# Optimization experiments

Hardware: AMD Instinct MI355X
Metric: run time of the kernel (lower is better)

The kernel has to match this reference:

```python
import jax, jax.numpy as jnp
import numpy as np

B, IN, OUT = 131072, 128, 32
GRID_SIZE, SPLINE_ORDER = 5, 3
GRID_LO, GRID_HI = -1.0, 1.0
N_BASIS = GRID_SIZE + SPLINE_ORDER  # 8


def _centers_and_spacing():
    n_knots = GRID_SIZE + 2 * SPLINE_ORDER + 1  # 12
    grid = jnp.linspace(GRID_LO, GRID_HI, n_knots)
    centers = grid[SPLINE_ORDER:SPLINE_ORDER + N_BASIS]  # (8,)
    spacing = (GRID_HI - GRID_LO) / GRID_SIZE + 1e-06
    return centers, spacing


def setup_inputs() -> dict:
    key = jax.random.key(0)
    k1, k2, k3 = jax.random.split(key, 3)
    x = jax.random.normal(k1, (B, IN), dtype=jnp.float32)
    coeff = jax.random.normal(k2, (IN, OUT, N_BASIS), dtype=jnp.float32) * 0.1
    base_weight = jnp.ones((IN, OUT), dtype=jnp.float32)
    base_bias = jnp.zeros((IN, OUT), dtype=jnp.float32)
    edge_weights = jax.random.normal(k3, (IN, OUT), dtype=jnp.float32) * 0.1
    return {"x": x, "coeff": coeff, "base_weight": base_weight,
            "base_bias": base_bias, "edge_weights": edge_weights}


def reference(x, coeff, base_weight, base_bias, edge_weights):
    # y[b,j] = sum_i w[i,j] * ( bw[i,j]*silu(x[b,i]) + bb[i,j]
    #                           + sum_k basis[b,i,k]*coeff[i,j,k] )
    centers, spacing = _centers_and_spacing()
    silu = x * jax.nn.sigmoid(x)                                    # (B, I)
    z = (x[:, :, None] - centers[None, None, :]) / spacing          # (B, I, K)
    basis = jnp.exp(-0.5 * z * z)                                   # (B, I, K)
    # base activation contribution
    base_out = jnp.einsum('bi,ij->bj', silu, edge_weights * base_weight)
    bias_out = jnp.sum(edge_weights * base_bias, axis=0)            # (J,)
    # spline contribution: contract over input dim i and basis dim k
    spline_out = jnp.einsum('bik,ijk->bj', basis,
                            edge_weights[:, :, None] * coeff)
    return base_out + bias_out[None, :] + spline_out
```

## Files before the change

kernel.cpp:

```cpp
#include <hip/hip_runtime.h>

typedef short bf16x8 __attribute__((ext_vector_type(8)));
typedef float f32x4v __attribute__((ext_vector_type(4)));

constexpr double H_D    = 0.4 + 1e-6;
constexpr double INVH_D = 1.0 / H_D;
constexpr double C0_D   = -1.0 + 6.0 / 11.0;
constexpr double DLT_D  = (2.0 / 11.0) / H_D;
constexpr double L2E_D  = 1.4426950408889634;

constexpr float INVH = (float)INVH_D;
constexpr float NC0H = (float)(-C0_D * INVH_D);
constexpr float A2f  = (float)(-0.5 * L2E_D);
constexpr float B2f  = (float)(DLT_D * L2E_D);
constexpr float GCF  = (float)(-0.5 * DLT_D * DLT_D * L2E_D);
constexpr float NL2E = (float)(-L2E_D);

__device__ __forceinline__ float fexp2(float v) {
#if __has_builtin(__builtin_amdgcn_exp2f)
  return __builtin_amdgcn_exp2f(v);
#else
  return exp2f(v);
#endif
}
__device__ __forceinline__ float frcp(float v) {
#if __has_builtin(__builtin_amdgcn_rcpf)
  return __builtin_amdgcn_rcpf(v);
#else
  return 1.0f / v;
#endif
}
__device__ __forceinline__ float siluf(float v) {
  return v * frcp(1.0f + fexp2(NL2E * v));
}
__device__ __forceinline__ unsigned pk2(float lo, float hi) {
  unsigned a = __float_as_uint(hi) + 0x8000u;
  unsigned b = __float_as_uint(lo) + 0x8000u;
  return __builtin_amdgcn_perm(a, b, 0x07060302u);
}
__device__ __forceinline__ bf16x8 packfrag(const float (&v)[8]) {
  uint4 d;
  d.x = pk2(v[0], v[1]);
  d.y = pk2(v[2], v[3]);
  d.z = pk2(v[4], v[5]);
  d.w = pk2(v[6], v[7]);
  return __builtin_bit_cast(bf16x8, d);
}
__device__ __forceinline__ unsigned rne16(float f) {
  unsigned u = __float_as_uint(f);
  return (u + 0x7fffu + ((u >> 16) & 1u)) >> 16;
}

__global__ void kan_prep(const float* __restrict__ coeff,
                         const float* __restrict__ bw,
                         const float* __restrict__ bb,
                         const float* __restrict__ ew,
                         uint4* __restrict__ wfrag,
                         float* __restrict__ bias) {
  if (blockIdx.x == 18) {
    int n = threadIdx.x;
    if (n < 32) {
      float s = 0.f;
      for (int i = 0; i < 128; ++i) s += ew[i * 32 + n] * bb[i * 32 + n];
      bias[n] = s;
    }
    return;
  }
  const int e    = blockIdx.x * 4 + (threadIdx.x >> 6);
  const int lane = threadIdx.x & 63;
  const int s = e >> 1, h = e & 1;
  const int G = s / 9, t = s % 9;
  const int n = h * 16 + (lane & 15);
  const int cbase = G * 32 + (lane >> 4) * 8;
  float v[8];
  if (t == 0) {
#pragma unroll
    for (int j = 0; j < 8; ++j) {
      int i = cbase + j;
      v[j] = ew[i * 32 + n] * bw[i * 32 + n];
    }
  } else {
    const int k = t - 1;
    const float g = exp2f(GCF * (float)(k * k));
#pragma unroll
    for (int j = 0; j < 8; ++j) {
      int i = cbase + j;
      v[j] = ew[i * 32 + n] * coeff[(i * 32 + n) * 8 + k] * g;
    }
  }
  uint4 d;
  d.x = (rne16(v[1]) << 16) | rne16(v[0]);
  d.y = (rne16(v[3]) << 16) | rne16(v[2]);
  d.z = (rne16(v[5]) << 16) | rne16(v[4]);
  d.w = (rne16(v[7]) << 16) | rne16(v[6]);
  wfrag[e * 64 + lane] = d;
}

__global__ __launch_bounds__(256, 2) void kan_main(
    const float* __restrict__ x,
    const uint4* __restrict__ wfrag,
    const float* __restrict__ bias,
    float* __restrict__ out) {
  const int lane = threadIdx.x & 63;
  const int wave = threadIdx.x >> 6;
  const int m    = lane & 15;
  const int quad = lane >> 4;
  const long rowbase = ((long)blockIdx.x * 4 + wave) * 64;

  f32x4v acc[4][2];
#pragma unroll
  for (int tl = 0; tl < 4; ++tl)
#pragma unroll
    for (int hh = 0; hh < 2; ++hh)
#pragma unroll
      for (int rr = 0; rr < 4; ++rr) acc[tl][hh][rr] = 0.f;

  const float* xbase = x + (long)m * 128 + quad * 8;

#pragma unroll
  for (int G = 0; G < 4; ++G) {
    const uint4* wf = wfrag + (size_t)G * 18 * 64 + lane;

    float xc[4][8];
#pragma unroll
    for (int tl = 0; tl < 4; ++tl) {
      const float4* p = reinterpret_cast<const float4*>(
          xbase + (rowbase + tl * 16) * 128 + G * 32);
      float4 a = p[0], b = p[1];
      xc[tl][0] = a.x; xc[tl][1] = a.y; xc[tl][2] = a.z; xc[tl][3] = a.w;
      xc[tl][4] = b.x; xc[tl][5] = b.y; xc[tl][6] = b.z; xc[tl][7] = b.w;
    }

    bf16x8 b0 = __builtin_bit_cast(bf16x8, wf[0]);
    bf16x8 b1 = __builtin_bit_cast(bf16x8, wf[64]);
#pragma unroll
    for (int tl = 0; tl < 4; ++tl) {
      float sv[8];
#pragma unroll
      for (int j = 0; j < 8; ++j) sv[j] = siluf(xc[tl][j]);
      bf16x8 af = packfrag(sv);
      acc[tl][0] = __builtin_amdgcn_mfma_f32_16x16x32_bf16(af, b0, acc[tl][0], 0, 0, 0);
      acc[tl][1] = __builtin_amdgcn_mfma_f32_16x16x32_bf16(af, b1, acc[tl][1], 0, 0, 0);
    }

    float pg[4][8], rg[4][8];
#pragma unroll
    for (int tl = 0; tl < 4; ++tl)
#pragma unroll
      for (int j = 0; j < 8; ++j) {
        float u = fmaf(xc[tl][j], INVH, NC0H);
        pg[tl][j] = fexp2(A2f * u * u);
        rg[tl][j] = fexp2(B2f * u);
      }

#pragma unroll
    for (int t = 1; t <= 8; ++t) {
      bf16x8 c0 = __builtin_bit_cast(bf16x8, wf[(t * 2) * 64]);
      bf16x8 c1 = __builtin_bit_cast(bf16x8, wf[(t * 2 + 1) * 64]);
#pragma unroll
      for (int tl = 0; tl < 4; ++tl) {
        bf16x8 af = packfrag(pg[tl]);
        acc[tl][0] = __builtin_amdgcn_mfma_f32_16x16x32_bf16(af, c0, acc[tl][0], 0, 0, 0);
        acc[tl][1] = __builtin_amdgcn_mfma_f32_16x16x32_bf16(af, c1, acc[tl][1], 0, 0, 0);
        if (t < 8) {
#pragma unroll
          for (int j = 0; j < 8; ++j) pg[tl][j] *= rg[tl][j];
        }
      }
    }
  }

  const float bv0 = bias[m];
  const float bv1 = bias[m + 16];
#pragma unroll
  for (int tl = 0; tl < 4; ++tl) {
#pragma unroll
    for (int rr = 0; rr < 4; ++rr) {
      long row = rowbase + tl * 16 + quad * 4 + rr;
      out[row * 32 + m]      = acc[tl][0][rr] + bv0;
      out[row * 32 + m + 16] = acc[tl][1][rr] + bv1;
    }
  }
}

extern "C" void kernel_launch(void* const* d_in, const int* in_sizes, int n_in,
                              void* d_out, int out_size, void* d_ws, size_t ws_size,
                              hipStream_t stream) {
  const float* x     = (const float*)d_in[0];
  const float* coeff = (const float*)d_in[1];
  const float* bw    = (const float*)d_in[2];
  const float* bb    = (const float*)d_in[3];
  const float* ew    = (const float*)d_in[4];

  uint4* wfrag = (uint4*)d_ws;
  float* bias  = (float*)((char*)d_ws + 73728);

  kan_prep<<<19, 256, 0, stream>>>(coeff, bw, bb, ew, wfrag, bias);
  kan_main<<<512, 256, 0, stream>>>(x, wfrag, bias, (float*)d_out);
}
```

Measured before the change: 127.5 us.

## Halve rows per wave, double grid, raise occupancy and prefetch next x chunk

Each wave now handles 32 rows instead of 64, the grid doubles to 1024 blocks, and launch bounds ask for 4 blocks per CU. The next group's x values are loaded into registers while the current group's MFMAs run. This targets load latency and low occupancy from the large per-thread register footprint. The cost is that each B weight fragment is reused across fewer row tiles, so weight loads per row double.

```diff
diff --git a/kernel.cpp b/kernel.cpp
--- a/kernel.cpp
+++ b/kernel.cpp
@@ -96,7 +96,7 @@
   wfrag[e * 64 + lane] = d;
 }
 
-__global__ __launch_bounds__(256, 2) void kan_main(
+__global__ __launch_bounds__(256, 4) void kan_main(
     const float* __restrict__ x,
     const uint4* __restrict__ wfrag,
     const float* __restrict__ bias,
@@ -105,60 +105,73 @@
   const int wave = threadIdx.x >> 6;
   const int m    = lane & 15;
   const int quad = lane >> 4;
-  const long rowbase = ((long)blockIdx.x * 4 + wave) * 64;
-
-  f32x4v acc[4][2];
-#pragma unroll
-  for (int tl = 0; tl < 4; ++tl)
+  const long rowbase = ((long)blockIdx.x * 4 + wave) * 32;
+
+  f32x4v acc[2][2];
+#pragma unroll
+  for (int tl = 0; tl < 2; ++tl)
 #pragma unroll
     for (int hh = 0; hh < 2; ++hh)
 #pragma unroll
       for (int rr = 0; rr < 4; ++rr) acc[tl][hh][rr] = 0.f;
 
-  const float* xbase = x + (long)m * 128 + quad * 8;
+  const float* xbase = x + (rowbase + m) * 128 + (long)quad * 8;
+
+  float xb[2][8];
+#pragma unroll
+  for (int tl = 0; tl < 2; ++tl) {
+    const float4* p =
+        reinterpret_cast<const float4*>(xbase + (long)tl * 16 * 128);
+    float4 a = p[0], b = p[1];
+    xb[tl][0] = a.x; xb[tl][1] = a.y; xb[tl][2] = a.z; xb[tl][3] = a.w;
+    xb[tl][4] = b.x; xb[tl][5] = b.y; xb[tl][6] = b.z; xb[tl][7] = b.w;
+  }
 
 #pragma unroll
   for (int G = 0; G < 4; ++G) {
     const uint4* wf = wfrag + (size_t)G * 18 * 64 + lane;
 
-    float xc[4][8];
-#pragma unroll
-    for (int tl = 0; tl < 4; ++tl) {
-      const float4* p = reinterpret_cast<const float4*>(
-          xbase + (rowbase + tl * 16) * 128 + G * 32);
-      float4 a = p[0], b = p[1];
-      xc[tl][0] = a.x; xc[tl][1] = a.y; xc[tl][2] = a.z; xc[tl][3] = a.w;
-      xc[tl][4] = b.x; xc[tl][5] = b.y; xc[tl][6] = b.z; xc[tl][7] = b.w;
-    }
-
-    bf16x8 b0 = __builtin_bit_cast(bf16x8, wf[0]);
-    bf16x8 b1 = __builtin_bit_cast(bf16x8, wf[64]);
-#pragma unroll
-    for (int tl = 0; tl < 4; ++tl) {
+    bf16x8 af0[2];
+    float pg[2][8], rg[2][8];
+#pragma unroll
+    for (int tl = 0; tl < 2; ++tl) {
       float sv[8];
 #pragma unroll
-      for (int j = 0; j < 8; ++j) sv[j] = siluf(xc[tl][j]);
-      bf16x8 af = packfrag(sv);
-      acc[tl][0] = __builtin_amdgcn_mfma_f32_16x16x32_bf16(af, b0, acc[tl][0], 0, 0, 0);
-      acc[tl][1] = __builtin_amdgcn_mfma_f32_16x16x32_bf16(af, b1, acc[tl][1], 0, 0, 0);
-    }
-
-    float pg[4][8], rg[4][8];
-#pragma unroll
-    for (int tl = 0; tl < 4; ++tl)
+      for (int j = 0; j < 8; ++j) sv[j] = siluf(xb[tl][j]);
+      af0[tl] = packfrag(sv);
 #pragma unroll
       for (int j = 0; j < 8; ++j) {
-        float u = fmaf(xc[tl][j], INVH, NC0H);
+        float u = fmaf(xb[tl][j], INVH, NC0H);
         pg[tl][j] = fexp2(A2f * u * u);
         rg[tl][j] = fexp2(B2f * u);
       }
+    }
+
+    if (G < 3) {
+#pragma unroll
+      for (int tl = 0; tl < 2; ++tl) {
+        const float4* p = reinterpret_cast<const float4*>(
+            xbase + (long)tl * 16 * 128 + (G + 1) * 32);
+        float4 a = p[0], b = p[1];
+        xb[tl][0] = a.x; xb[tl][1] = a.y; xb[tl][2] = a.z; xb[tl][3] = a.w;
+        xb[tl][4] = b.x; xb[tl][5] = b.y; xb[tl][6] = b.z; xb[tl][7] = b.w;
+      }
+    }
+
+    bf16x8 b0 = __builtin_bit_cast(bf16x8, wf[0]);
+    bf16x8 b1 = __builtin_bit_cast(bf16x8, wf[64]);
+#pragma unroll
+    for (int tl = 0; tl < 2; ++tl) {
+      acc[tl][0] = __builtin_amdgcn_mfma_f32_16x16x32_bf16(af0[tl], b0, acc[tl][0], 0, 0, 0);
+      acc[tl][1] = __builtin_amdgcn_mfma_f32_16x16x32_bf16(af0[tl], b1, acc[tl][1], 0, 0, 0);
+    }
 
 #pragma unroll
     for (int t = 1; t <= 8; ++t) {
       bf16x8 c0 = __builtin_bit_cast(bf16x8, wf[(t * 2) * 64]);
       bf16x8 c1 = __builtin_bit_cast(bf16x8, wf[(t * 2 + 1) * 64]);
 #pragma unroll
-      for (int tl = 0; tl < 4; ++tl) {
+      for (int tl = 0; tl < 2; ++tl) {
         bf16x8 af = packfrag(pg[tl]);
         acc[tl][0] = __builtin_amdgcn_mfma_f32_16x16x32_bf16(af, c0, acc[tl][0], 0, 0, 0);
         acc[tl][1] = __builtin_amdgcn_mfma_f32_16x16x32_bf16(af, c1, acc[tl][1], 0, 0, 0);
@@ -173,7 +186,7 @@
   const float bv0 = bias[m];
   const float bv1 = bias[m + 16];
 #pragma unroll
-  for (int tl = 0; tl < 4; ++tl) {
+  for (int tl = 0; tl < 2; ++tl) {
 #pragma unroll
     for (int rr = 0; rr < 4; ++rr) {
       long row = rowbase + tl * 16 + quad * 4 + rr;
@@ -196,5 +209,5 @@
   float* bias  = (float*)((char*)d_ws + 73728);
 
   kan_prep<<<19, 256, 0, stream>>>(coeff, bw, bb, ew, wfrag, bias);
-  kan_main<<<512, 256, 0, stream>>>(x, wfrag, bias, (float*)d_out);
-}
+  kan_main<<<1024, 256, 0, stream>>>(x, wfrag, bias, (float*)d_out);
+}
```

After: 121.7 us. -4.6%, faster.

## Stage weight fragments in LDS and shrink per-wave tile to raise occupancy

Applied to the files above, without the earlier changes.

The main kernel now gives each wave 16 rows instead of 64, launches four times as many blocks, and raises the launch bound to 8 blocks per SM. Each block copies the weight fragments for every input group into LDS with global_load_lds, and the next group's x values are prefetched while the current group is computed. The aim is more latency hiding through occupancy, and cheaper weight reads from LDS than repeated global reads. The cost is a barrier per group and weights reloaded by four times as many blocks, with less MFMA reuse of each weight fragment per wave. The bias reduction in the prep kernel is also parallelised across 256 threads.

```diff
diff --git a/kernel.cpp b/kernel.cpp
--- a/kernel.cpp
+++ b/kernel.cpp
@@ -58,11 +58,20 @@
                          uint4* __restrict__ wfrag,
                          float* __restrict__ bias) {
   if (blockIdx.x == 18) {
-    int n = threadIdx.x;
-    if (n < 32) {
-      float s = 0.f;
-      for (int i = 0; i < 128; ++i) s += ew[i * 32 + n] * bb[i * 32 + n];
-      bias[n] = s;
+    __shared__ float part[256];
+    const int n = threadIdx.x & 31;
+    const int c = threadIdx.x >> 5;
+    float s = 0.f;
+#pragma unroll
+    for (int i = c * 16; i < c * 16 + 16; ++i)
+      s += ew[i * 32 + n] * bb[i * 32 + n];
+    part[threadIdx.x] = s;
+    __syncthreads();
+    if (threadIdx.x < 32) {
+      float t = 0.f;
+#pragma unroll
+      for (int c2 = 0; c2 < 8; ++c2) t += part[c2 * 32 + threadIdx.x];
+      bias[threadIdx.x] = t;
     }
     return;
   }
@@ -96,90 +105,99 @@
   wfrag[e * 64 + lane] = d;
 }
 
-__global__ __launch_bounds__(256, 2) void kan_main(
+__device__ __forceinline__ void gl_lds16(const uint4* g, uint4* l) {
+  __builtin_amdgcn_global_load_lds(
+      (const __attribute__((address_space(1))) void*)g,
+      (__attribute__((address_space(3))) void*)l, 16, 0, 0);
+}
+
+__global__ __launch_bounds__(256, 8) void kan_main(
     const float* __restrict__ x,
     const uint4* __restrict__ wfrag,
     const float* __restrict__ bias,
     float* __restrict__ out) {
-  const int lane = threadIdx.x & 63;
-  const int wave = threadIdx.x >> 6;
+  __shared__ uint4 wlds[1152];
+  const int tid  = threadIdx.x;
+  const int lane = tid & 63;
+  const int wave = tid >> 6;
   const int m    = lane & 15;
   const int quad = lane >> 4;
-  const long rowbase = ((long)blockIdx.x * 4 + wave) * 64;
-
-  f32x4v acc[4][2];
-#pragma unroll
-  for (int tl = 0; tl < 4; ++tl)
-#pragma unroll
-    for (int hh = 0; hh < 2; ++hh)
-#pragma unroll
-      for (int rr = 0; rr < 4; ++rr) acc[tl][hh][rr] = 0.f;
-
-  const float* xbase = x + (long)m * 128 + quad * 8;
-
-#pragma unroll
-  for (int G = 0; G < 4; ++G) {
-    const uint4* wf = wfrag + (size_t)G * 18 * 64 + lane;
-
-    float xc[4][8];
-#pragma unroll
-    for (int tl = 0; tl < 4; ++tl) {
-      const float4* p = reinterpret_cast<const float4*>(
-          xbase + (rowbase + tl * 16) * 128 + G * 32);
-      float4 a = p[0], b = p[1];
-      xc[tl][0] = a.x; xc[tl][1] = a.y; xc[tl][2] = a.z; xc[tl][3] = a.w;
-      xc[tl][4] = b.x; xc[tl][5] = b.y; xc[tl][6] = b.z; xc[tl][7] = b.w;
-    }
-
-    bf16x8 b0 = __builtin_bit_cast(bf16x8, wf[0]);
-    bf16x8 b1 = __builtin_bit_cast(bf16x8, wf[64]);
-#pragma unroll
-    for (int tl = 0; tl < 4; ++tl) {
-      float sv[8];
-#pragma unroll
-      for (int j = 0; j < 8; ++j) sv[j] = siluf(xc[tl][j]);
-      bf16x8 af = packfrag(sv);
-      acc[tl][0] = __builtin_amdgcn_mfma_f32_16x16x32_bf16(af, b0, acc[tl][0], 0, 0, 0);
-      acc[tl][1] = __builtin_amdgcn_mfma_f32_16x16x32_bf16(af, b1, acc[tl][1], 0, 0, 0);
-    }
-
-    float pg[4][8], rg[4][8];
-#pragma unroll
-    for (int tl = 0; tl < 4; ++tl)
-#pragma unroll
-      for (int j = 0; j < 8; ++j) {
-        float u = fmaf(xc[tl][j], INVH, NC0H);
-        pg[tl][j] = fexp2(A2f * u * u);
-        rg[tl][j] = fexp2(B2f * u);
-      }
-
-#pragma unroll
-    for (int t = 1; t <= 8; ++t) {
-      bf16x8 c0 = __builtin_bit_cast(bf16x8, wf[(t * 2) * 64]);
-      bf16x8 c1 = __builtin_bit_cast(bf16x8, wf[(t * 2 + 1) * 64]);
-#pragma unroll
-      for (int tl = 0; tl < 4; ++tl) {
-        bf16x8 af = packfrag(pg[tl]);
-        acc[tl][0] = __builtin_amdgcn_mfma_f32_16x16x32_bf16(af, c0, acc[tl][0], 0, 0, 0);
-        acc[tl][1] = __builtin_amdgcn_mfma_f32_16x16x32_bf16(af, c1, acc[tl][1], 0, 0, 0);
-        if (t < 8) {
-#pragma unroll
-          for (int j = 0; j < 8; ++j) pg[tl][j] *= rg[tl][j];
-        }
-      }
-    }
-  }
-
+  const long rowbase = ((long)blockIdx.x * 4 + wave) * 16;
+
+  f32x4v acc0, acc1;
+#pragma unroll
+  for (int rr = 0; rr < 4; ++rr) { acc0[rr] = 0.f; acc1[rr] = 0.f; }
+
+  const float* xbase = x + (rowbase + m) * 128 + (long)quad * 8;
+
+  float xb[8];
+  {
+    const float4* p = reinterpret_cast<const float4*>(xbase);
+    float4 a = p[0], b = p[1];
+    xb[0] = a.x; xb[1] = a.y; xb[2] = a.z; xb[3] = a.w;
+    xb[4] = b.x; xb[5] = b.y; xb[6] = b.z; xb[7] = b.w;
+  }
   const float bv0 = bias[m];
   const float bv1 = bias[m + 16];
-#pragma unroll
-  for (int tl = 0; tl < 4; ++tl) {
-#pragma unroll
-    for (int rr = 0; rr < 4; ++rr) {
-      long row = rowbase + tl * 16 + quad * 4 + rr;
-      out[row * 32 + m]      = acc[tl][0][rr] + bv0;
-      out[row * 32 + m + 16] = acc[tl][1][rr] + bv1;
-    }
+
+#pragma unroll 1
+  for (int G = 0; G < 4; ++G) {
+    if (G) __syncthreads();
+    const uint4* src = wfrag + (size_t)G * 1152;
+#pragma unroll
+    for (int i = 0; i < 4; ++i)
+      gl_lds16(src + tid + i * 256, &wlds[tid + i * 256]);
+    if (tid < 128) gl_lds16(src + 1024 + tid, &wlds[1024 + tid]);
+    __syncthreads();
+
+    bf16x8 af0;
+    float pg[8], rg[8];
+    {
+      float sv[8];
+#pragma unroll
+      for (int j = 0; j < 8; ++j) sv[j] = siluf(xb[j]);
+      af0 = packfrag(sv);
+#pragma unroll
+      for (int j = 0; j < 8; ++j) {
+        float u = fmaf(xb[j], INVH, NC0H);
+        pg[j] = fexp2(A2f * u * u);
+        rg[j] = fexp2(B2f * u);
+      }
+    }
+
+    if (G < 3) {
+      const float4* p = reinterpret_cast<const float4*>(xbase + (G + 1) * 32);
+      float4 a = p[0], b = p[1];
+      xb[0] = a.x; xb[1] = a.y; xb[2] = a.z; xb[3] = a.w;
+      xb[4] = b.x; xb[5] = b.y; xb[6] = b.z; xb[7] = b.w;
+    }
+
+    const uint4* wl = wlds + lane;
+
+    acc0 = __builtin_amdgcn_mfma_f32_16x16x32_bf16(
+        af0, __builtin_bit_cast(bf16x8, wl[0]), acc0, 0, 0, 0);
+    acc1 = __builtin_amdgcn_mfma_f32_16x16x32_bf16(
+        af0, __builtin_bit_cast(bf16x8, wl[64]), acc1, 0, 0, 0);
+
+#pragma unroll
+    for (int t = 1; t <= 8; ++t) {
+      bf16x8 c0 = __builtin_bit_cast(bf16x8, wl[t * 128]);
+      bf16x8 c1 = __builtin_bit_cast(bf16x8, wl[t * 128 + 64]);
+      bf16x8 af = packfrag(pg);
+      acc0 = __builtin_amdgcn_mfma_f32_16x16x32_bf16(af, c0, acc0, 0, 0, 0);
+      acc1 = __builtin_amdgcn_mfma_f32_16x16x32_bf16(af, c1, acc1, 0, 0, 0);
+      if (t < 8) {
+#pragma unroll
+        for (int j = 0; j < 8; ++j) pg[j] *= rg[j];
+      }
+    }
+  }
+
+#pragma unroll
+  for (int rr = 0; rr < 4; ++rr) {
+    long row = rowbase + quad * 4 + rr;
+    out[row * 32 + m]      = acc0[rr] + bv0;
+    out[row * 32 + m + 16] = acc1[rr] + bv1;
   }
 }
 
@@ -196,5 +214,5 @@
   float* bias  = (float*)((char*)d_ws + 73728);
 
   kan_prep<<<19, 256, 0, stream>>>(coeff, bw, bb, ew, wfrag, bias);
-  kan_main<<<512, 256, 0, stream>>>(x, wfrag, bias, (float*)d_out);
-}
+  kan_main<<<2048, 256, 0, stream>>>(x, wfrag, bias, (float*)d_out);
+}
```

After: 116.3 us. 8.8% less time.
